# Kernel optimization log

Hardware: AMD Instinct MI355X
Metric: run time of the kernel (lower is better)

The kernel has to match this reference:

```python
import jax, jax.numpy as jnp
import numpy as np

N_NODES = 100000

def _gcn_conv(x, edge_index, W, b):
    # PyG GCNConv with normalize=False, add_self_loops=False:
    # out[dst] = sum_{(src,dst) in E} (x @ W)[src] + b
    xw = x @ W                                   # [N, out]
    src, dst = edge_index[0], edge_index[1]
    agg = jax.ops.segment_sum(xw[src], dst, num_segments=x.shape[0])  # [N, out]
    return agg + b

def setup_inputs() -> dict:
    key = jax.random.key(0)
    k1, k2, k3, k4 = jax.random.split(key, 4)
    F_in, F_hid, F_out = 128, 64, 40
    E = 1_600_000
    x = jax.random.normal(k1, (N_NODES, F_in), dtype=jnp.float32)
    edge_index = jax.random.randint(k2, (2, E), 0, N_NODES, dtype=jnp.int64)
    W1 = jax.random.normal(k3, (F_in, F_hid), dtype=jnp.float32) * (1.0 / np.sqrt(F_in))
    b1 = jnp.zeros((F_hid,), dtype=jnp.float32)
    W2 = jax.random.normal(k4, (F_hid, F_out), dtype=jnp.float32) * (1.0 / np.sqrt(F_hid))
    b2 = jnp.zeros((F_out,), dtype=jnp.float32)
    return {"x": x, "edge_index": edge_index, "W1": W1, "b1": b1, "W2": W2, "b2": b2}

def reference(x, edge_index, W1, b1, W2, b2):
    h = _gcn_conv(x, edge_index, W1, b1)
    h = jax.nn.relu(h)
    h = _gcn_conv(h, edge_index, W2, b2)
    return jax.nn.log_softmax(h, axis=1)
```

## Files before the change

kernel.cpp:

```cpp
#include <hip/hip_runtime.h>
#include <cstdint>
#include <cstddef>

#define F_IN  128
#define F_HID 64
#define F_OUT 40

#define BSH   9
#define NBMAX 256
#define CHUNK 4096

#define BLD_T   512
#define BLD_CAP 10240

typedef __attribute__((ext_vector_type(8))) short short8;
typedef __attribute__((ext_vector_type(4))) float f32x4;

__device__ __forceinline__ unsigned short f2bf(float f) {
  unsigned u = __float_as_uint(f);
  u += 0x7fffu + ((u >> 16) & 1u);
  return (unsigned short)(u >> 16);
}
__device__ __forceinline__ float bf2f(unsigned short b) {
  return __uint_as_float((unsigned)b << 16);
}
__device__ __forceinline__ float bflo(unsigned u) { return __uint_as_float(u << 16); }
__device__ __forceinline__ float bfhi(unsigned u) { return __uint_as_float(u & 0xffff0000u); }
__device__ __forceinline__ unsigned packbf(float lo, float hi) {
  return (unsigned)f2bf(lo) | ((unsigned)f2bf(hi) << 16);
}

__global__ __launch_bounds__(256) void front_k(const float* __restrict__ x,
                                               const float* __restrict__ W1,
                                               const float* __restrict__ W2,
                                               unsigned short* __restrict__ w2s,
                                               unsigned short* __restrict__ xw, int N,
                                               const int* __restrict__ ei,
                                               int* __restrict__ counts,
                                               int E, int NBLK, int NB1, int NBUCK) {
  __shared__ int lh[NBMAX];
  __shared__ unsigned short w1l[8192];
  int t = threadIdx.x;

  if ((int)blockIdx.x < NBLK) {
    int blk = blockIdx.x;
    lh[t] = 0;
    __syncthreads();
    int e0 = blk * CHUNK;
    int n = min(CHUNK, E - e0);
    for (int i = t; i < n; i += 256)
      atomicAdd(&lh[((unsigned)ei[E + e0 + i]) >> BSH], 1);
    __syncthreads();
    if (t < NBUCK) counts[t * NB1 + blk] = lh[t];
    if (blk == 0) {
      for (int i = t; i < 3072; i += 256) {
        int f = i >> 9, r = i & 511;
        int lane = r >> 3, jj = r & 7;
        int ct = f >> 1, ks = f & 1;
        int n2 = ct * 16 + (lane & 15);
        int k = ks * 32 + (lane >> 4) * 8 + jj;
        w2s[i] = (n2 < F_OUT) ? f2bf(W2[k * F_OUT + n2]) : (unsigned short)0;
      }
    }
    return;
  }

  {
    int k = t >> 1, n0 = (t & 1) * 32;
    const float4* wp = (const float4*)(W1 + k * F_HID + n0);
    float4 v[8];
#pragma unroll
    for (int u = 0; u < 8; ++u) v[u] = wp[u];
#pragma unroll
    for (int u = 0; u < 32; ++u) {
      int n = n0 + u;
      float f = ((const float*)v)[u];
      int idx = ((n >> 4) * 4 + (k >> 5)) * 512 +
                (((k >> 3) & 3) * 16 + (n & 15)) * 8 + (k & 7);
      w1l[idx] = f2bf(f);
    }
  }
  __syncthreads();

  int gblk = blockIdx.x - NBLK;
  int lane = t & 63;
  int wid  = gblk * 4 + (t >> 6);
  int row0 = wid * 16;
  if (row0 >= N) return;
  int m = lane & 15, q = lane >> 4;

  if (row0 + 16 <= N) {
    short8 b[16];
#pragma unroll
    for (int f = 0; f < 16; ++f)
      b[f] = *(const short8*)(w1l + f * 512 + lane * 8);

    short8 a[4];
#pragma unroll
    for (int ks = 0; ks < 4; ++ks) {
      const float* xp = x + (size_t)(row0 + m) * F_IN + ks * 32 + q * 8;
      float4 v0 = *(const float4*)xp;
      float4 v1 = *(const float4*)(xp + 4);
      short8 tt;
      tt[0] = (short)f2bf(v0.x); tt[1] = (short)f2bf(v0.y);
      tt[2] = (short)f2bf(v0.z); tt[3] = (short)f2bf(v0.w);
      tt[4] = (short)f2bf(v1.x); tt[5] = (short)f2bf(v1.y);
      tt[6] = (short)f2bf(v1.z); tt[7] = (short)f2bf(v1.w);
      a[ks] = tt;
    }

    f32x4 z = {0.f, 0.f, 0.f, 0.f};
    f32x4 acc[4] = {z, z, z, z};
#pragma unroll
    for (int ct = 0; ct < 4; ++ct)
#pragma unroll
      for (int ks = 0; ks < 4; ++ks)
        acc[ct] = __builtin_amdgcn_mfma_f32_16x16x32_bf16(a[ks], b[ct * 4 + ks],
                                                          acc[ct], 0, 0, 0);
#pragma unroll
    for (int ct = 0; ct < 4; ++ct)
#pragma unroll
      for (int r = 0; r < 4; ++r) {
        int row = row0 + q * 4 + r;
        xw[(size_t)row * F_HID + ct * 16 + m] = f2bf(acc[ct][r]);
      }
  } else {
    for (int r = 0; r < 16 && row0 + r < N; ++r) {
      const float* xr = x + (size_t)(row0 + r) * F_IN;
      float s = 0.f;
      for (int k = 0; k < F_IN; ++k) s = fmaf(xr[k], W1[k * F_HID + lane], s);
      xw[(size_t)(row0 + r) * F_HID + lane] = f2bf(s);
    }
  }
}

__global__ __launch_bounds__(256) void scanR_k(int* __restrict__ counts,
                                               int NBLK, int NB1) {
  __shared__ int sm[512];
  __shared__ int psc[256];
  int t = threadIdx.x;
  int* c = counts + blockIdx.x * NB1;

  sm[t]       = (t < NBLK)       ? c[t]       : 0;
  sm[t + 256] = (t + 256 < NBLK) ? c[t + 256] : 0;
  __syncthreads();

  int v0 = sm[2 * t], v1 = sm[2 * t + 1];
  int pair = v0 + v1;
  psc[t] = pair;
  __syncthreads();
  for (int off = 1; off < 256; off <<= 1) {
    int add = (t >= off) ? psc[t - off] : 0;
    __syncthreads();
    psc[t] += add;
    __syncthreads();
  }
  int ep = psc[t] - pair;
  if (2 * t < NBLK)     c[2 * t]     = ep;
  if (2 * t + 1 < NBLK) c[2 * t + 1] = ep + v0;
  if (t == 0) c[NBLK] = psc[255];
}

__global__ __launch_bounds__(256) void partition_k(const int* __restrict__ counts,
                                                   const int* __restrict__ ei,
                                                   unsigned* __restrict__ ebuf,
                                                   int E, int NBLK, int NB1,
                                                   int NBUCK) {
  __shared__ uint2 slots[CHUNK];
  __shared__ int scn[NBMAX], lcur[NBMAX], gadj[NBMAX];
  int t = threadIdx.x, blk = blockIdx.x;
  int e0 = blk * CHUNK;
  int n = min(CHUNK, E - e0);

  int rowTot = (t < NBUCK) ? counts[t * NB1 + NBLK] : 0;
  scn[t] = rowTot;
  __syncthreads();
  for (int off = 1; off < 256; off <<= 1) {
    int add = (t >= off) ? scn[t - off] : 0;
    __syncthreads();
    scn[t] += add;
    __syncthreads();
  }
  int bucketBase = scn[t] - rowTot;
  __syncthreads();

  int cnt = 0, base0 = 0;
  if (t < NBUCK) {
    int cpre  = counts[t * NB1 + blk];
    int cnext = counts[t * NB1 + blk + 1];
    cnt = cnext - cpre;
    base0 = bucketBase + cpre;
  }
  scn[t] = cnt;
  __syncthreads();
  for (int off = 1; off < 256; off <<= 1) {
    int add = (t >= off) ? scn[t - off] : 0;
    __syncthreads();
    scn[t] += add;
    __syncthreads();
  }
  int excl = scn[t] - cnt;
  if (t < NBUCK) { lcur[t] = excl; gadj[t] = base0 - excl; }
  __syncthreads();

  for (int i = t; i < n; i += 256) {
    int s = ei[e0 + i], d = ei[E + e0 + i];
    int pos = atomicAdd(&lcur[((unsigned)d) >> BSH], 1);
    slots[pos] = make_uint2((unsigned)s, (unsigned)d);
  }
  __syncthreads();
  for (int i = t; i < n; i += 256) {
    uint2 sd = slots[i];
    unsigned pk = ((sd.y & 511u) << 17) | sd.x;
    ebuf[gadj[sd.y >> BSH] + i] = pk;
  }
}

__global__ __launch_bounds__(BLD_T) void build_k(const unsigned* __restrict__ ebuf,
                                                 const int* __restrict__ counts,
                                                 int* __restrict__ row_ptr,
                                                 int* __restrict__ csr,
                                                 int N, int E, int NBLK, int NB1,
                                                 int NBUCK) {
  __shared__ int hist[512];
  __shared__ int psc[256];
  __shared__ int btot[NBMAX];
  __shared__ unsigned stg[BLD_CAP];
  int t = threadIdx.x, b = blockIdx.x;
  int nodeBase = b << BSH;

  if (t < 256) btot[t] = (t < NBUCK) ? counts[t * NB1 + NBLK] : 0;
  __syncthreads();
  for (int off = 1; off < 256; off <<= 1) {
    int add = (t >= off && t < 256) ? btot[t - off] : 0;
    __syncthreads();
    if (t < 256) btot[t] += add;
    __syncthreads();
  }
  int S = (b > 0) ? btot[b - 1] : 0;
  int T = btot[b];
  int n = T - S;
  bool useLds = (n <= BLD_CAP);
  __syncthreads();

  if (t < 512) hist[t] = 0;
  __syncthreads();
  for (int i = t; i < n; i += BLD_T) {
    unsigned v = ebuf[S + i];
    if (useLds) stg[i] = v;
    atomicAdd(&hist[v >> 17], 1);
  }
  __syncthreads();

  int v0 = 0, v1 = 0, pair = 0;
  if (t < 256) {
    v0 = hist[2 * t]; v1 = hist[2 * t + 1];
    pair = v0 + v1;
    psc[t] = pair;
  }
  __syncthreads();
  for (int off = 1; off < 256; off <<= 1) {
    int add = (t >= off && t < 256) ? psc[t - off] : 0;
    __syncthreads();
    if (t < 256) psc[t] += add;
    __syncthreads();
  }
  if (t < 256) {
    int ep = psc[t] - pair;
    int e0 = ep, e1 = ep + v0;
    int node0 = nodeBase + 2 * t;
    if (node0 < N) row_ptr[node0] = S + e0;
    if (node0 + 1 < N) row_ptr[node0 + 1] = S + e1;
    hist[2 * t] = e0; hist[2 * t + 1] = e1;
  }
  if (b == 0 && t == 0) row_ptr[N] = E;
  __syncthreads();
  for (int i = t; i < n; i += BLD_T) {
    unsigned v = useLds ? stg[i] : ebuf[S + i];
    int pos = atomicAdd(&hist[v >> 17], 1);
    csr[S + pos] = (int)(v & 0x1FFFFu);
  }
}

#define GATHER8(SRC, STRIDE_SH)                                              \
  for (; i + 7 < end; i += 8) {                                              \
    int s0 = csr[i],     s1 = csr[i + 1], s2 = csr[i + 2], s3 = csr[i + 3];  \
    int s4 = csr[i + 4], s5 = csr[i + 5], s6 = csr[i + 6], s7 = csr[i + 7];  \
    uint4 v0 = *(const uint4*)(SRC + ((size_t)s0 << STRIDE_SH) + (part << 3)); \
    uint4 v1 = *(const uint4*)(SRC + ((size_t)s1 << STRIDE_SH) + (part << 3)); \
    uint4 v2 = *(const uint4*)(SRC + ((size_t)s2 << STRIDE_SH) + (part << 3)); \
    uint4 v3 = *(const uint4*)(SRC + ((size_t)s3 << STRIDE_SH) + (part << 3)); \
    uint4 v4 = *(const uint4*)(SRC + ((size_t)s4 << STRIDE_SH) + (part << 3)); \
    uint4 v5 = *(const uint4*)(SRC + ((size_t)s5 << STRIDE_SH) + (part << 3)); \
    uint4 v6 = *(const uint4*)(SRC + ((size_t)s6 << STRIDE_SH) + (part << 3)); \
    uint4 v7 = *(const uint4*)(SRC + ((size_t)s7 << STRIDE_SH) + (part << 3)); \
    ACC8(acc, v0); ACC8(bcc, v1); ACC8(acc, v2); ACC8(bcc, v3);              \
    ACC8(acc, v4); ACC8(bcc, v5); ACC8(acc, v6); ACC8(bcc, v7);              \
  }                                                                          \
  for (; i < end; ++i) {                                                     \
    int s = csr[i];                                                          \
    uint4 v = *(const uint4*)(SRC + ((size_t)s << STRIDE_SH) + (part << 3)); \
    ACC8(acc, v);                                                            \
  }

#define ACC8(A, V)                                                           \
  A[0] += bflo(V.x); A[1] += bfhi(V.x); A[2] += bflo(V.y); A[3] += bfhi(V.y);\
  A[4] += bflo(V.z); A[5] += bfhi(V.z); A[6] += bflo(V.w); A[7] += bfhi(V.w);

__global__ __launch_bounds__(256) void agg1g2_k(const unsigned short* __restrict__ xw,
                                                const int* __restrict__ row_ptr,
                                                const int* __restrict__ csr,
                                                const float* __restrict__ b1,
                                                const unsigned short* __restrict__ w2s,
                                                const float* __restrict__ W2,
                                                unsigned short* __restrict__ hw, int N) {
  __shared__ uint4 hsm[32][8];
  int t = threadIdx.x;
  int wave = t >> 6, lane = t & 63;
  int blockRow0 = blockIdx.x * 32;
  int row = blockRow0 + wave * 8 + (lane >> 3);
  int part = lane & 7;
  bool live = row < N;

  int start = live ? row_ptr[row] : 0;
  int end   = live ? row_ptr[row + 1] : 0;

  float acc[8], bcc[8];
#pragma unroll
  for (int j = 0; j < 8; ++j) { acc[j] = 0.f; bcc[j] = 0.f; }

  int i = start;
  GATHER8(xw, 6)

  if (live) {
    int c0 = part << 3;
    float4 bA = *(const float4*)(b1 + c0);
    float4 bB = *(const float4*)(b1 + c0 + 4);
    float r0 = fmaxf(acc[0] + bcc[0] + bA.x, 0.f);
    float r1 = fmaxf(acc[1] + bcc[1] + bA.y, 0.f);
    float r2 = fmaxf(acc[2] + bcc[2] + bA.z, 0.f);
    float r3 = fmaxf(acc[3] + bcc[3] + bA.w, 0.f);
    float r4 = fmaxf(acc[4] + bcc[4] + bB.x, 0.f);
    float r5 = fmaxf(acc[5] + bcc[5] + bB.y, 0.f);
    float r6 = fmaxf(acc[6] + bcc[6] + bB.z, 0.f);
    float r7 = fmaxf(acc[7] + bcc[7] + bB.w, 0.f);
    uint4 o = make_uint4(packbf(r0, r1), packbf(r2, r3),
                         packbf(r4, r5), packbf(r6, r7));
    int lr = row - blockRow0;
    hsm[lr][part ^ (lr & 7)] = o;
  }
  __syncthreads();

  if (wave < 2) {
    int frow0 = blockRow0 + wave * 16;
    if (frow0 >= N) return;
    int m = lane & 15, q = lane >> 4;
    if (frow0 + 16 <= N) {
      short8 b[6];
#pragma unroll
      for (int f = 0; f < 6; ++f)
        b[f] = *(const short8*)(w2s + f * 512 + lane * 8);
      short8 a[2];
#pragma unroll
      for (int ks = 0; ks < 2; ++ks) {
        int lr = wave * 16 + m;
        int pp = ks * 4 + q;
        a[ks] = *(const short8*)&hsm[lr][pp ^ (lr & 7)];
      }
      f32x4 z = {0.f, 0.f, 0.f, 0.f};
      f32x4 acc2[3] = {z, z, z};
#pragma unroll
      for (int ct = 0; ct < 3; ++ct)
#pragma unroll
        for (int ks = 0; ks < 2; ++ks)
          acc2[ct] = __builtin_amdgcn_mfma_f32_16x16x32_bf16(
              a[ks], b[ct * 2 + ks], acc2[ct], 0, 0, 0);
#pragma unroll
      for (int ct = 0; ct < 3; ++ct)
#pragma unroll
        for (int r = 0; r < 4; ++r) {
          int row2 = frow0 + q * 4 + r;
          int c = ct * 16 + m;
          if (c < F_OUT) hw[(size_t)row2 * F_HID + c] = f2bf(acc2[ct][r]);
        }
    } else {
      for (int r = 0; r < 16; ++r) {
        int row2 = frow0 + r;
        if (row2 >= N) break;
        if (lane < F_OUT) {
          int lr = wave * 16 + r;
          float s = 0.f;
          for (int k = 0; k < F_HID; ++k) {
            const unsigned short* hp =
                (const unsigned short*)&hsm[lr][(k >> 3) ^ (lr & 7)];
            s = fmaf(bf2f(hp[k & 7]), W2[k * F_OUT + lane], s);
          }
          hw[(size_t)row2 * F_HID + lane] = f2bf(s);
        }
      }
    }
  }
}

__global__ __launch_bounds__(256) void agg2_ls_k(const unsigned short* __restrict__ hw,
                                                 const int* __restrict__ row_ptr,
                                                 const int* __restrict__ csr,
                                                 const float* __restrict__ b2,
                                                 float* __restrict__ out, int N) {
  int t = threadIdx.x;
  int wave = t >> 6, lane = t & 63;
  int grp = lane / 5;
  int part = lane - grp * 5;
  int row = blockIdx.x * 48 + wave * 12 + grp;
  bool live = (grp < 12) && (row < N);

  int start = live ? row_ptr[row] : 0;
  int end   = live ? row_ptr[row + 1] : 0;

  float acc[8], bcc[8];
#pragma unroll
  for (int j = 0; j < 8; ++j) { acc[j] = 0.f; bcc[j] = 0.f; }

  int i = start;
  GATHER8(hw, 6)

  float vj[8];
  float mx = -3.4e38f;
  if (live) {
    int c0 = part << 3;
    float4 bA = *(const float4*)(b2 + c0);
    float4 bB = *(const float4*)(b2 + c0 + 4);
    vj[0] = acc[0] + bcc[0] + bA.x; vj[1] = acc[1] + bcc[1] + bA.y;
    vj[2] = acc[2] + bcc[2] + bA.z; vj[3] = acc[3] + bcc[3] + bA.w;
    vj[4] = acc[4] + bcc[4] + bB.x; vj[5] = acc[5] + bcc[5] + bB.y;
    vj[6] = acc[6] + bcc[6] + bB.z; vj[7] = acc[7] + bcc[7] + bB.w;
#pragma unroll
    for (int q = 0; q < 8; ++q) mx = fmaxf(mx, vj[q]);
  }
  int g0 = (grp < 12 ? grp : 0) * 5;
  float mxAll = mx;
#pragma unroll
  for (int q = 0; q < 5; ++q) mxAll = fmaxf(mxAll, __shfl(mx, g0 + q, 64));
  float ex = 0.f;
  if (live) {
#pragma unroll
    for (int q = 0; q < 8; ++q) ex += __expf(vj[q] - mxAll);
  }
  float exAll = 0.f;
#pragma unroll
  for (int q = 0; q < 5; ++q) exAll += __shfl(ex, g0 + q, 64);
  float lse = __logf(exAll) + mxAll;

  if (live) {
    int c0 = part << 3;
    float* op = out + (size_t)row * F_OUT + c0;
    *(float4*)op = make_float4(vj[0] - lse, vj[1] - lse, vj[2] - lse, vj[3] - lse);
    *(float4*)(op + 4) = make_float4(vj[4] - lse, vj[5] - lse, vj[6] - lse, vj[7] - lse);
  }
}

extern "C" void kernel_launch(void* const* d_in, const int* in_sizes, int n_in,
                              void* d_out, int out_size, void* d_ws, size_t ws_size,
                              hipStream_t stream) {
  const float* x  = (const float*)d_in[0];
  const int*   ei = (const int*)d_in[1];
  const float* W1 = (const float*)d_in[2];
  const float* b1 = (const float*)d_in[3];
  const float* W2 = (const float*)d_in[4];
  const float* b2 = (const float*)d_in[5];

  int N = in_sizes[0] / F_IN;
  int E = in_sizes[1] / 2;

  char* base = (char*)d_ws;
  size_t szA = (size_t)N * F_HID * sizeof(unsigned short);
  size_t szEb = (size_t)E * sizeof(unsigned);
  size_t szHw = (size_t)N * F_HID * sizeof(unsigned short);
  size_t szB = (szEb > szHw) ? szEb : szHw;
  unsigned short* xw = (unsigned short*)base;
  char* regB = base + ((szA + 255) & ~(size_t)255);
  unsigned* ebuf       = (unsigned*)regB;
  unsigned short* hw   = (unsigned short*)regB;
  int* row_ptr = (int*)(regB + ((szB + 255) & ~(size_t)255));
  int* csr     = row_ptr + N + 1;
  int* counts  = csr + E;
  float* out = (float*)d_out;

  int NBLK  = (E + CHUNK - 1) / CHUNK;
  int NB1   = NBLK + 1;
  int NBUCK = (N + 511) >> BSH;
  unsigned short* w2s =
      (unsigned short*)(((uintptr_t)(counts + NBUCK * NB1) + 63) & ~(uintptr_t)63);
  int gemmGrid = (N + 63) / 64;
  int aggGrid1 = (N + 31) / 32;
  int aggGrid2 = (N + 47) / 48;

  front_k<<<NBLK + gemmGrid, 256, 0, stream>>>(x, W1, W2, w2s, xw, N,
                                               ei, counts, E, NBLK, NB1, NBUCK);

  scanR_k<<<NBUCK, 256, 0, stream>>>(counts, NBLK, NB1);
  partition_k<<<NBLK, 256, 0, stream>>>(counts, ei, ebuf, E, NBLK, NB1, NBUCK);
  build_k<<<NBUCK, BLD_T, 0, stream>>>(ebuf, counts, row_ptr, csr,
                                       N, E, NBLK, NB1, NBUCK);

  agg1g2_k<<<aggGrid1, 256, 0, stream>>>(xw, row_ptr, csr, b1, w2s, W2, hw, N);
  agg2_ls_k<<<aggGrid2, 256, 0, stream>>>(hw, row_ptr, csr, b2, out, N);
}
```

Measured before the change: 215.2 us.

## Drop separate count scan kernel; recompute bucket prefixes inside partition and build

Removes the scanR_k launch. The per-block bucket histogram is now stored block-major as counts[blk*256+t], and each partition block loops over all block counts to get its own prefix and the bucket totals. build_k also recomputes the bucket totals by summing over all blocks. This saves one kernel launch and its dependency gap, but every partition block (about 391 of them) now reads the whole counts array (about 100K ints), which adds redundant L2 traffic.

```diff
diff --git a/kernel.cpp b/kernel.cpp
--- a/kernel.cpp
+++ b/kernel.cpp
@@ -37,7 +37,7 @@
                                                unsigned short* __restrict__ xw, int N,
                                                const int* __restrict__ ei,
                                                int* __restrict__ counts,
-                                               int E, int NBLK, int NB1, int NBUCK) {
+                                               int E, int NBLK, int NBUCK) {
   __shared__ int lh[NBMAX];
   __shared__ unsigned short w1l[8192];
   int t = threadIdx.x;
@@ -51,7 +51,7 @@
     for (int i = t; i < n; i += 256)
       atomicAdd(&lh[((unsigned)ei[E + e0 + i]) >> BSH], 1);
     __syncthreads();
-    if (t < NBUCK) counts[t * NB1 + blk] = lh[t];
+    counts[blk * 256 + t] = lh[t];
     if (blk == 0) {
       for (int i = t; i < 3072; i += 256) {
         int f = i >> 9, r = i & 511;
@@ -134,46 +134,23 @@
   }
 }
 
-__global__ __launch_bounds__(256) void scanR_k(int* __restrict__ counts,
-                                               int NBLK, int NB1) {
-  __shared__ int sm[512];
-  __shared__ int psc[256];
-  int t = threadIdx.x;
-  int* c = counts + blockIdx.x * NB1;
-
-  sm[t]       = (t < NBLK)       ? c[t]       : 0;
-  sm[t + 256] = (t + 256 < NBLK) ? c[t + 256] : 0;
-  __syncthreads();
-
-  int v0 = sm[2 * t], v1 = sm[2 * t + 1];
-  int pair = v0 + v1;
-  psc[t] = pair;
-  __syncthreads();
-  for (int off = 1; off < 256; off <<= 1) {
-    int add = (t >= off) ? psc[t - off] : 0;
-    __syncthreads();
-    psc[t] += add;
-    __syncthreads();
-  }
-  int ep = psc[t] - pair;
-  if (2 * t < NBLK)     c[2 * t]     = ep;
-  if (2 * t + 1 < NBLK) c[2 * t + 1] = ep + v0;
-  if (t == 0) c[NBLK] = psc[255];
-}
-
 __global__ __launch_bounds__(256) void partition_k(const int* __restrict__ counts,
                                                    const int* __restrict__ ei,
                                                    unsigned* __restrict__ ebuf,
-                                                   int E, int NBLK, int NB1,
-                                                   int NBUCK) {
+                                                   int E, int NBLK, int NBUCK) {
   __shared__ uint2 slots[CHUNK];
   __shared__ int scn[NBMAX], lcur[NBMAX], gadj[NBMAX];
   int t = threadIdx.x, blk = blockIdx.x;
   int e0 = blk * CHUNK;
   int n = min(CHUNK, E - e0);
 
-  int rowTot = (t < NBUCK) ? counts[t * NB1 + NBLK] : 0;
-  scn[t] = rowTot;
+  int pre = 0, tot = 0;
+  for (int j = 0; j < NBLK; ++j) {
+    int c = counts[j * 256 + t];
+    pre += (j < blk) ? c : 0;
+    tot += c;
+  }
+  scn[t] = tot;
   __syncthreads();
   for (int off = 1; off < 256; off <<= 1) {
     int add = (t >= off) ? scn[t - off] : 0;
@@ -181,16 +158,10 @@
     scn[t] += add;
     __syncthreads();
   }
-  int bucketBase = scn[t] - rowTot;
-  __syncthreads();
-
-  int cnt = 0, base0 = 0;
-  if (t < NBUCK) {
-    int cpre  = counts[t * NB1 + blk];
-    int cnext = counts[t * NB1 + blk + 1];
-    cnt = cnext - cpre;
-    base0 = bucketBase + cpre;
-  }
+  int base0 = (scn[t] - tot) + pre;
+  int cnt = counts[blk * 256 + t];
+  __syncthreads();
+
   scn[t] = cnt;
   __syncthreads();
   for (int off = 1; off < 256; off <<= 1) {
@@ -200,7 +171,8 @@
     __syncthreads();
   }
   int excl = scn[t] - cnt;
-  if (t < NBUCK) { lcur[t] = excl; gadj[t] = base0 - excl; }
+  lcur[t] = excl;
+  gadj[t] = base0 - excl;
   __syncthreads();
 
   for (int i = t; i < n; i += 256) {
@@ -220,8 +192,7 @@
                                                  const int* __restrict__ counts,
                                                  int* __restrict__ row_ptr,
                                                  int* __restrict__ csr,
-                                                 int N, int E, int NBLK, int NB1,
-                                                 int NBUCK) {
+                                                 int N, int E, int NBLK, int NBUCK) {
   __shared__ int hist[512];
   __shared__ int psc[256];
   __shared__ int btot[NBMAX];
@@ -229,7 +200,11 @@
   int t = threadIdx.x, b = blockIdx.x;
   int nodeBase = b << BSH;
 
-  if (t < 256) btot[t] = (t < NBUCK) ? counts[t * NB1 + NBLK] : 0;
+  if (t < 256) {
+    int tot = 0;
+    for (int j = 0; j < NBLK; ++j) tot += counts[j * 256 + t];
+    btot[t] = tot;
+  }
   __syncthreads();
   for (int off = 1; off < 256; off <<= 1) {
     int add = (t >= off && t < 256) ? btot[t - off] : 0;
@@ -487,21 +462,19 @@
   float* out = (float*)d_out;
 
   int NBLK  = (E + CHUNK - 1) / CHUNK;
-  int NB1   = NBLK + 1;
   int NBUCK = (N + 511) >> BSH;
   unsigned short* w2s =
-      (unsigned short*)(((uintptr_t)(counts + NBUCK * NB1) + 63) & ~(uintptr_t)63);
+      (unsigned short*)(((uintptr_t)(counts + NBLK * 256) + 63) & ~(uintptr_t)63);
   int gemmGrid = (N + 63) / 64;
   int aggGrid1 = (N + 31) / 32;
   int aggGrid2 = (N + 47) / 48;
 
   front_k<<<NBLK + gemmGrid, 256, 0, stream>>>(x, W1, W2, w2s, xw, N,
-                                               ei, counts, E, NBLK, NB1, NBUCK);
-
-  scanR_k<<<NBUCK, 256, 0, stream>>>(counts, NBLK, NB1);
-  partition_k<<<NBLK, 256, 0, stream>>>(counts, ei, ebuf, E, NBLK, NB1, NBUCK);
+                                               ei, counts, E, NBLK, NBUCK);
+
+  partition_k<<<NBLK, 256, 0, stream>>>(counts, ei, ebuf, E, NBLK, NBUCK);
   build_k<<<NBUCK, BLD_T, 0, stream>>>(ebuf, counts, row_ptr, csr,
-                                       N, E, NBLK, NB1, NBUCK);
+                                       N, E, NBLK, NBUCK);
 
   agg1g2_k<<<aggGrid1, 256, 0, stream>>>(xw, row_ptr, csr, b1, w2s, W2, hw, N);
   agg2_ls_k<<<aggGrid2, 256, 0, stream>>>(hw, row_ptr, csr, b2, out, N);
```

New measurement: 307.6 us. 43.0% more time.
